# Kernel tuning notes

Hardware: AMD Instinct MI355X
Metric: run time of the kernel (lower is better)

Reference implementation:

```python
import jax, jax.numpy as jnp
import numpy as np

N, P, E, D, OUT = 4096, 2048, 65536, 1024, 128


def _lin(k, fin, fout):
    kw, kb = jax.random.split(k)
    s = 1.0 / np.sqrt(fin)
    return (jax.random.uniform(kw, (fin, fout), jnp.float32, -s, s),
            jax.random.uniform(kb, (fout,), jnp.float32, -s, s))


def setup_inputs() -> dict:
    key = jax.random.key(0)
    ks = jax.random.split(key, 16)
    inst_feat = jax.random.normal(ks[0], (N, D), jnp.float32)
    phra_feat = jax.random.normal(ks[1], (P, D), jnp.float32)
    # unique (subject, object) pairs: the original overwrites duplicates in connection_marker
    pair_ids = jax.random.choice(ks[2], N * N, (E,), replace=False)
    conn_mat = jnp.stack([pair_ids // N, pair_ids % N]).astype(jnp.int32)  # [2, E]
    # every phrase id appears -> exist_phra_id == arange(P), matching original indexing
    phra_clu_idx = jax.random.permutation(ks[3], jnp.arange(E, dtype=jnp.int32) % P)
    p_s_W, p_s_b = _lin(ks[4], 2 * D, OUT)
    s_p_W, s_p_b = _lin(ks[5], 2 * D, OUT)
    p_o_W, p_o_b = _lin(ks[6], 2 * D, OUT)
    o_p_W, o_p_b = _lin(ks[7], 2 * D, OUT)
    inst_w1_W, inst_w1_b = _lin(ks[8], D, D)
    inst_w2_W, inst_w2_b = _lin(ks[9], D, D)
    phra_w1_W, phra_w1_b = _lin(ks[10], D, D)
    phra_w2_W, phra_w2_b = _lin(ks[11], D, D)
    return dict(inst_feat=inst_feat, phra_feat=phra_feat, conn_mat=conn_mat,
                phra_clu_idx=phra_clu_idx,
                p_s_W=p_s_W, p_s_b=p_s_b, p_o_W=p_o_W, p_o_b=p_o_b,
                o_p_W=o_p_W, o_p_b=o_p_b, s_p_W=s_p_W, s_p_b=s_p_b,
                inst_w1_W=inst_w1_W, inst_w1_b=inst_w1_b,
                inst_w2_W=inst_w2_W, inst_w2_b=inst_w2_b,
                phra_w1_W=phra_w1_W, phra_w1_b=phra_w1_b,
                phra_w2_W=phra_w2_W, phra_w2_b=phra_w2_b)


def _gated_msg(src, tgt, W, b):
    # MassageGenerator: gate = sigmoid(relu([src; tgt] @ W + b)).mean(1); msg = src * gate
    gate = jax.nn.sigmoid(jax.nn.relu(jnp.concatenate([src, tgt], axis=1) @ W + b)).mean(axis=1)
    return src * gate[:, None]


def _seg_mean(x, seg, num_segments):
    s = jax.ops.segment_sum(x, seg, num_segments=num_segments)
    c = jax.ops.segment_sum(jnp.ones((x.shape[0],), x.dtype), seg, num_segments=num_segments)
    return s / jnp.maximum(c, 1.0)[:, None]  # zeros where no edges == padded msg


def _refine(msg, tar, w1_W, w1_b, w2_W, w2_b):
    # MassageApply: out = input1 + relu(w1(input1)) + relu(w2(input2)); input1 = summed msg
    return msg + jax.nn.relu(msg @ w1_W + w1_b) + jax.nn.relu(tar @ w2_W + w2_b)


def reference(inst_feat, phra_feat, conn_mat, phra_clu_idx,
              p_s_W, p_s_b, p_o_W, p_o_b, o_p_W, o_p_b, s_p_W, s_p_b,
              inst_w1_W, inst_w1_b, inst_w2_W, inst_w2_b,
              phra_w1_W, phra_w1_b, phra_w2_W, phra_w2_b):
    s_idx, o_idx = conn_mat[0], conn_mat[1]
    subj_f = inst_feat[s_idx]          # [E, D]
    obj_f = inst_feat[o_idx]           # [E, D]
    phr_f = phra_feat[phra_clu_idx]    # [E, D]
    n, p = inst_feat.shape[0], phra_feat.shape[0]
    # phrase -> subject / object messages, mean over each node's incident edges
    p_s = _seg_mean(_gated_msg(phr_f, subj_f, p_s_W, p_s_b), s_idx, n)
    p_o = _seg_mean(_gated_msg(phr_f, obj_f, p_o_W, p_o_b), o_idx, n)
    # object / subject -> phrase messages, mean over edges sharing a cluster id
    o_p = _seg_mean(_gated_msg(obj_f, phr_f, o_p_W, o_p_b), phra_clu_idx, p)
    s_p = _seg_mean(_gated_msg(subj_f, phr_f, s_p_W, s_p_b), phra_clu_idx, p)
    inst_out = _refine((p_o + p_s) * 0.5, inst_feat, inst_w1_W, inst_w1_b, inst_w2_W, inst_w2_b)
    phra_out = _refine((o_p + s_p) * 0.5, phra_feat, phra_w1_W, phra_w1_b, phra_w2_W, phra_w2_b)
    return inst_out, phra_out
```

## Files before the change

kernel.cpp:

```cpp
#include <hip/hip_runtime.h>
#include <math.h>

constexpr int NN  = 4096;
constexpr int PP  = 2048;
constexpr int EE  = 65536;
constexpr int DD  = 1024;
constexpr int OUTF = 128;
constexpr int G4  = 512;

typedef __attribute__((ext_vector_type(8))) short short8v;
typedef __attribute__((ext_vector_type(4))) float f32x4;

__device__ __forceinline__ float sigmoid_relu(float z) {
    z = fmaxf(z, 0.0f);
    return 1.0f / (1.0f + __expf(-z));
}
__device__ __forceinline__ float b2f(ushort u) {
    return __uint_as_float(((unsigned int)u) << 16);
}
__device__ __forceinline__ ushort f2b(float f) {
    unsigned int x = __float_as_uint(f);
    return (ushort)((x + 0x7fffu + ((x >> 16) & 1u)) >> 16);
}
__device__ __forceinline__ unsigned int pack2(float a, float b) {
    return (unsigned int)f2b(a) | ((unsigned int)f2b(b) << 16);
}

#define GLD16(gptr, lptr) \
    __builtin_amdgcn_global_load_lds((__attribute__((address_space(1))) const void*)(gptr), \
                                     (__attribute__((address_space(3))) void*)(lptr), 16, 0, 0)
#define ASM_VMCNT(n) asm volatile("s_waitcnt vmcnt(" #n ")" ::: "memory")
#define BARRIER() do { asm volatile("" ::: "memory"); \
                       __builtin_amdgcn_s_barrier();  \
                       asm volatile("" ::: "memory"); } while (0)

constexpr int NCNT    = 2 * (NN + NN + PP);
constexpr int NB_ZERO = NCNT / 256;
constexpr int NB_F2B  = (NN + PP) * DD / 4 / 256;
constexpr int NB_PACK = G4 * DD / 256;
constexpr int NB_WT   = 4 * (DD / 64) * (DD / 64);

__global__ __launch_bounds__(256) void prep_kernel(
        int* __restrict__ cntBlock,
        const float* __restrict__ instF, const float* __restrict__ phraF,
        ushort* __restrict__ instB, ushort* __restrict__ phraB,
        const float* __restrict__ psW, const float* __restrict__ poW,
        const float* __restrict__ opW, const float* __restrict__ spW,
        const float* __restrict__ psB, const float* __restrict__ poB,
        const float* __restrict__ opB, const float* __restrict__ spB,
        ushort* __restrict__ WiT, ushort* __restrict__ WpT,
        float* __restrict__ biascat,
        const float* __restrict__ W0, const float* __restrict__ W1,
        const float* __restrict__ W2, const float* __restrict__ W3,
        ushort* __restrict__ T0, ushort* __restrict__ T1,
        ushort* __restrict__ T2, ushort* __restrict__ T3) {
    __shared__ float tile[64][65];
    int b = blockIdx.x, t = threadIdx.x;
    if (b < NB_ZERO) {
        cntBlock[b * 256 + t] = 0;
        return;
    }
    b -= NB_ZERO;
    if (b < NB_F2B) {
        int i = b * 256 + t;
        constexpr int na4 = NN * DD / 4;
        if (i < na4) {
            float4 v = ((const float4*)instF)[i];
            ushort4 u; u.x = f2b(v.x); u.y = f2b(v.y); u.z = f2b(v.z); u.w = f2b(v.w);
            ((ushort4*)instB)[i] = u;
        } else {
            int j = i - na4;
            float4 v = ((const float4*)phraF)[j];
            ushort4 u; u.x = f2b(v.x); u.y = f2b(v.y); u.z = f2b(v.z); u.w = f2b(v.w);
            ((ushort4*)phraB)[j] = u;
        }
        return;
    }
    b -= NB_F2B;
    if (b < NB_PACK) {
        int idx = b * 256 + t;
        int n = idx >> 10, k = idx & 1023;
        int g = n >> 7, j = n & 127;
        float wi, wp;
        if (g == 0)      { wi = psW[(size_t)(DD + k) * OUTF + j]; wp = psW[(size_t)k * OUTF + j]; }
        else if (g == 1) { wi = poW[(size_t)(DD + k) * OUTF + j]; wp = poW[(size_t)k * OUTF + j]; }
        else if (g == 2) { wi = opW[(size_t)k * OUTF + j];        wp = opW[(size_t)(DD + k) * OUTF + j]; }
        else             { wi = spW[(size_t)k * OUTF + j];        wp = spW[(size_t)(DD + k) * OUTF + j]; }
        WiT[idx] = f2b(wi);
        WpT[idx] = f2b(wp);
        if (idx < G4) {
            int gg = idx >> 7, jj = idx & 127;
            biascat[idx] = (gg == 0) ? psB[jj] : (gg == 1) ? poB[jj]
                         : (gg == 2) ? opB[jj] : spB[jj];
        }
        return;
    }
    b -= NB_PACK;
    int z = b >> 8, rest = b & 255;
    const float* W = (z == 0) ? W0 : (z == 1) ? W1 : (z == 2) ? W2 : W3;
    ushort*      T = (z == 0) ? T0 : (z == 1) ? T1 : (z == 2) ? T2 : T3;
    int k0 = (rest & 15) * 64, n0 = (rest >> 4) * 64;
    int tx = t & 63, ty = t >> 6;
    #pragma unroll
    for (int i = 0; i < 64; i += 4)
        tile[ty + i][tx] = W[(size_t)(k0 + ty + i) * DD + n0 + tx];
    __syncthreads();
    #pragma unroll
    for (int i = 0; i < 64; i += 4)
        T[(size_t)(n0 + ty + i) * DD + k0 + tx] = f2b(tile[tx][ty + i]);
}

template<int BROWS>
__device__ __forceinline__ void stage_tiles(const ushort* __restrict__ A,
                                            const ushort* __restrict__ BT,
                                            int bm, int bn, int k0,
                                            ushort* Asl, ushort* Bsl, int t) {
    #pragma unroll
    for (int r = 0; r < 4; r++) {
        int ch = r * 256 + t;
        int row = ch >> 3;
        int sw = ((ch & 7) ^ (row & 7)) << 3;
        GLD16(A + (size_t)(bm + row) * DD + k0 + sw, &Asl[ch * 8]);
    }
    #pragma unroll
    for (int r = 0; r < BROWS / 32; r++) {
        int ch = r * 256 + t;
        int row = ch >> 3;
        int sw = ((ch & 7) ^ (row & 7)) << 3;
        GLD16(BT + (size_t)(bn + row) * DD + k0 + sw, &Bsl[ch * 8]);
    }
}

template<int NACC>
__device__ __forceinline__ void compute_tiles(const ushort* Asl, const ushort* Bsl,
                                              f32x4 (&acc)[4][NACC],
                                              int wr, int wc, int lr, int lk) {
    #pragma unroll
    for (int kk = 0; kk < 2; kk++) {
        int ch16 = kk * 4 + lk;
        short8v a[4], b[NACC];
        #pragma unroll
        for (int m = 0; m < 4; m++) {
            int ra = wr + m * 16 + lr;
            a[m] = *(const short8v*)&Asl[ra * 64 + ((ch16 ^ (ra & 7)) << 3)];
        }
        #pragma unroll
        for (int n = 0; n < NACC; n++) {
            int rb = wc + n * 16 + lr;
            b[n] = *(const short8v*)&Bsl[rb * 64 + ((ch16 ^ (rb & 7)) << 3)];
        }
        #pragma unroll
        for (int m = 0; m < 4; m++)
            #pragma unroll
            for (int n = 0; n < NACC; n++)
                acc[m][n] = __builtin_amdgcn_mfma_f32_16x16x32_bf16(a[m], b[n], acc[m][n], 0, 0, 0);
    }
}

__global__ __launch_bounds__(256) void mfma_tables_kernel(
        const ushort* __restrict__ instB, const ushort* __restrict__ WiT,
        const ushort* __restrict__ phraB, const ushort* __restrict__ WpT,
        const float* __restrict__ biascat,
        ushort* __restrict__ TiB, ushort* __restrict__ TpB) {
    __shared__ ushort Asl[2][128 * 64];
    __shared__ ushort Bsl[2][64 * 64];
    int bx = blockIdx.x;
    const ushort *A, *BT; ushort* C; const float* bias;
    if (bx < NN / 128) { A = instB; BT = WiT; C = TiB; bias = nullptr; }
    else { bx -= NN / 128; A = phraB; BT = WpT; C = TpB; bias = biascat; }
    int bm = bx * 128, bn = blockIdx.y * 64;
    int t = threadIdx.x;
    const int lane = t & 63, w = t >> 6;
    const int wr = (w >> 1) * 64, wc = (w & 1) * 32;
    const int lr = lane & 15, lk = lane >> 4;
    f32x4 acc[4][2] = {};

    int cur = 0;
    stage_tiles<64>(A, BT, bm, bn, 0, Asl[0], Bsl[0], t);
    for (int k0 = 0; k0 < DD; k0 += 64) {
        int nxt = cur ^ 1;
        if (k0 + 64 < DD) {
            stage_tiles<64>(A, BT, bm, bn, k0 + 64, Asl[nxt], Bsl[nxt], t);
            ASM_VMCNT(6);
        } else {
            ASM_VMCNT(0);
        }
        BARRIER();
        compute_tiles<2>(Asl[cur], Bsl[cur], acc, wr, wc, lr, lk);
        BARRIER();
        cur = nxt;
    }
    #pragma unroll
    for (int m = 0; m < 4; m++) {
        int row = bm + wr + m * 16 + lk * 4;
        #pragma unroll
        for (int n = 0; n < 2; n++) {
            int col = bn + wc + n * 16 + lr;
            float bv = bias ? bias[col] : 0.f;
            #pragma unroll
            for (int r = 0; r < 4; r++)
                C[(size_t)(row + r) * G4 + col] = f2b(acc[m][n][r] + bv);
        }
    }
}

__global__ __launch_bounds__(256) void mfma_refine_kernel(
        const ushort* __restrict__ imsgB, const ushort* __restrict__ instB,
        const ushort* __restrict__ iw1T, const ushort* __restrict__ iw2T,
        const float* __restrict__ ib1, const float* __restrict__ ib2,
        float* __restrict__ iout,
        const ushort* __restrict__ pmsgB, const ushort* __restrict__ phraB,
        const ushort* __restrict__ pw1T, const ushort* __restrict__ pw2T,
        const float* __restrict__ pb1, const float* __restrict__ pb2,
        float* __restrict__ pout) {
    __shared__ ushort Asl[2][128 * 64];
    __shared__ ushort Bsl[2][64 * 64];
    int bx = blockIdx.x;
    const ushort *Am, *Af, *W1, *W2; const float *b1, *b2; float* out;
    if (bx < NN / 128) {
        Am = imsgB; Af = instB; W1 = iw1T; W2 = iw2T; b1 = ib1; b2 = ib2; out = iout;
    } else {
        bx -= NN / 128;
        Am = pmsgB; Af = phraB; W1 = pw1T; W2 = pw2T; b1 = pb1; b2 = pb2; out = pout;
    }
    int bm = bx * 128, bn = blockIdx.y * 64;
    int t = threadIdx.x;
    const int lane = t & 63, w = t >> 6;
    const int wr = (w >> 1) * 64, wc = (w & 1) * 32;
    const int lr = lane & 15, lk = lane >> 4;
    f32x4 acc1[4][2] = {};
    f32x4 acc2[4][2] = {};

    int cur = 0;
    stage_tiles<64>(Am, W1, bm, bn, 0, Asl[0], Bsl[0], t);
    auto run = [&](const ushort* A, const ushort* B, f32x4 (&acc)[4][2],
                   const ushort* An, const ushort* Bn) {
        for (int k0 = 0; k0 < DD; k0 += 64) {
            int nxt = cur ^ 1;
            if (k0 + 64 < DD) {
                stage_tiles<64>(A, B, bm, bn, k0 + 64, Asl[nxt], Bsl[nxt], t);
                ASM_VMCNT(6);
            } else if (An) {
                stage_tiles<64>(An, Bn, bm, bn, 0, Asl[nxt], Bsl[nxt], t);
                ASM_VMCNT(6);
            } else {
                ASM_VMCNT(0);
            }
            BARRIER();
            compute_tiles<2>(Asl[cur], Bsl[cur], acc, wr, wc, lr, lk);
            BARRIER();
            cur = nxt;
        }
    };
    run(Am, W1, acc1, Af, W2);
    run(Af, W2, acc2, nullptr, nullptr);

    #pragma unroll
    for (int m = 0; m < 4; m++) {
        int row = bm + wr + m * 16 + lk * 4;
        #pragma unroll
        for (int n = 0; n < 2; n++) {
            int col = bn + wc + n * 16 + lr;
            float vb1 = b1[col], vb2 = b2[col];
            #pragma unroll
            for (int r = 0; r < 4; r++) {
                float v = b2f(Am[(size_t)(row + r) * DD + col])
                        + fmaxf(acc1[m][n][r] + vb1, 0.f)
                        + fmaxf(acc2[m][n][r] + vb2, 0.f);
                out[(size_t)(row + r) * DD + col] = v;
            }
        }
    }
}

__global__ void hist_kernel(const int* __restrict__ s_idx, const int* __restrict__ o_idx,
                            const int* __restrict__ c_idx,
                            int* cntS, int* cntO, int* cntC) {
    int e = blockIdx.x * blockDim.x + threadIdx.x;
    if (e >= EE) return;
    atomicAdd(&cntS[s_idx[e]], 1);
    atomicAdd(&cntO[o_idx[e]], 1);
    atomicAdd(&cntC[c_idx[e]], 1);
}

__global__ __launch_bounds__(1024) void scan3_kernel(
        const int* __restrict__ cntS, const int* __restrict__ cntO,
        const int* __restrict__ cntC,
        int* __restrict__ startS, int* __restrict__ startO, int* __restrict__ startC) {
    const int* cnt; int* start; int n;
    if (blockIdx.x == 0)      { cnt = cntS; start = startS; n = NN; }
    else if (blockIdx.x == 1) { cnt = cntO; start = startO; n = NN; }
    else                      { cnt = cntC; start = startC; n = PP; }
    __shared__ int sh[1024];
    int t = threadIdx.x;
    int per = n >> 10;
    int base = t * per;
    int s = 0;
    for (int i = 0; i < per; i++) s += cnt[base + i];
    sh[t] = s;
    __syncthreads();
    for (int off = 1; off < 1024; off <<= 1) {
        int v = (t >= off) ? sh[t - off] : 0;
        __syncthreads();
        sh[t] += v;
        __syncthreads();
    }
    int ex = (t == 0) ? 0 : sh[t - 1];
    for (int i = 0; i < per; i++) { start[base + i] = ex; ex += cnt[base + i]; }
    if (t == 1023) start[n] = ex;
}

__global__ __launch_bounds__(256) void gate_kernel(
        const int* __restrict__ s_idx, const int* __restrict__ o_idx,
        const int* __restrict__ c_idx,
        const int* __restrict__ startS, const int* __restrict__ startO,
        const int* __restrict__ startC,
        int* __restrict__ curS, int* __restrict__ curO, int* __restrict__ curC,
        const ushort* __restrict__ Ti, const ushort* __restrict__ Tp,
        int2* __restrict__ pkS, int2* __restrict__ pkO, int4* __restrict__ pkC) {
    int gid = blockIdx.x * 256 + threadIdx.x;
    int e = gid >> 6, lane = gid & 63;
    if (e >= EE) return;
    int s = s_idx[e], o = o_idx[e], c = c_idx[e];
    const unsigned int* tpc = (const unsigned int*)(Tp + (size_t)c * G4);
    const unsigned int* tis = (const unsigned int*)(Ti + (size_t)s * G4);
    const unsigned int* tio = (const unsigned int*)(Ti + (size_t)o * G4);
    auto pairSig = [](unsigned int a, unsigned int b) {
        float lo = __uint_as_float(a << 16) + __uint_as_float(b << 16);
        float hi = __uint_as_float(a & 0xffff0000u) + __uint_as_float(b & 0xffff0000u);
        return sigmoid_relu(lo) + sigmoid_relu(hi);
    };
    float s0 = pairSig(tpc[lane],       tis[lane]);
    float s1 = pairSig(tpc[64 + lane],  tio[64 + lane]);
    float s2 = pairSig(tpc[128 + lane], tio[128 + lane]);
    float s3 = pairSig(tpc[192 + lane], tis[192 + lane]);
    #pragma unroll
    for (int off = 32; off; off >>= 1) {
        s0 += __shfl_xor(s0, off);
        s1 += __shfl_xor(s1, off);
        s2 += __shfl_xor(s2, off);
        s3 += __shfl_xor(s3, off);
    }
    if (lane == 0) {
        const float inv = 1.0f / 128.0f;
        int ps = startS[s] + atomicAdd(&curS[s], 1);
        int po = startO[o] + atomicAdd(&curO[o], 1);
        int pc = startC[c] + atomicAdd(&curC[c], 1);
        pkS[ps] = make_int2(c, __float_as_int(s0 * inv));
        pkO[po] = make_int2(c, __float_as_int(s1 * inv));
        pkC[pc] = make_int4(o, s, __float_as_int(s2 * inv), __float_as_int(s3 * inv));
    }
}

__device__ __forceinline__ void accum8(float* acc, uint4 v, float g) {
    acc[0] += g * __uint_as_float(v.x << 16);
    acc[1] += g * __uint_as_float(v.x & 0xffff0000u);
    acc[2] += g * __uint_as_float(v.y << 16);
    acc[3] += g * __uint_as_float(v.y & 0xffff0000u);
    acc[4] += g * __uint_as_float(v.z << 16);
    acc[5] += g * __uint_as_float(v.z & 0xffff0000u);
    acc[6] += g * __uint_as_float(v.w << 16);
    acc[7] += g * __uint_as_float(v.w & 0xffff0000u);
}

__global__ __launch_bounds__(256) void seg_kernel(
        const ushort* __restrict__ phraB, const ushort* __restrict__ instB,
        const int2* __restrict__ pkS, const int* __restrict__ startS,
        const int2* __restrict__ pkO, const int* __restrict__ startO,
        const int4* __restrict__ pkC, const int* __restrict__ startC,
        ushort* __restrict__ imsgB, ushort* __restrict__ pmsgB) {
    __shared__ float lds[4][64 * 17];
    int w = threadIdx.x >> 6, lane = threadIdx.x & 63;
    float acc[16];
    #pragma unroll
    for (int j = 0; j < 16; j++) acc[j] = 0.f;
    int bx = blockIdx.x;
    bool instSide = bx < NN / 2;
    int segB, segE;
    ushort* msgB;
    int base2;
    if (instSide) {
        int node = bx * 2 + (w >> 1);
        const int2* pk_list = (w & 1) ? pkO : pkS;
        const int*  start   = (w & 1) ? startO : startS;
        int b = start[node], e = start[node + 1];
        if (b < e) {
            int2 pk = pk_list[b];
            const uint4* r = (const uint4*)(phraB + (size_t)pk.x * DD) + lane;
            uint4 c0 = r[0], c1 = r[64];
            for (int i = b + 1; i < e; i++) {
                int2 pkn = pk_list[i];
                const uint4* rn = (const uint4*)(phraB + (size_t)pkn.x * DD) + lane;
                uint4 n0 = rn[0], n1 = rn[64];
                float g = __int_as_float(pk.y);
                accum8(acc, c0, g); accum8(acc + 8, c1, g);
                pk = pkn; c0 = n0; c1 = n1;
            }
            float g = __int_as_float(pk.y);
            accum8(acc, c0, g); accum8(acc + 8, c1, g);
        }
        segB = b; segE = e; msgB = imsgB; base2 = bx * 2;
    } else {
        int pbx = bx - NN / 2;
        int p = pbx * 2 + (w >> 1);
        int half = w & 1;
        int cb = startC[p], ce = startC[p + 1];
        int i0 = cb + half;
        if (i0 < ce) {
            int4 pk = pkC[i0];
            const uint4* ro = (const uint4*)(instB + (size_t)pk.x * DD) + lane;
            const uint4* rs = (const uint4*)(instB + (size_t)pk.y * DD) + lane;
            uint4 o0 = ro[0], o1 = ro[64], s0 = rs[0], s1 = rs[64];
            for (int i = i0 + 2; i < ce; i += 2) {
                int4 pkn = pkC[i];
                const uint4* rno = (const uint4*)(instB + (size_t)pkn.x * DD) + lane;
                const uint4* rns = (const uint4*)(instB + (size_t)pkn.y * DD) + lane;
                uint4 no0 = rno[0], no1 = rno[64], ns0 = rns[0], ns1 = rns[64];
                float go = __int_as_float(pk.z), gs = __int_as_float(pk.w);
                accum8(acc, o0, go); accum8(acc + 8, o1, go);
                accum8(acc, s0, gs); accum8(acc + 8, s1, gs);
                pk = pkn; o0 = no0; o1 = no1; s0 = ns0; s1 = ns1;
            }
            float go = __int_as_float(pk.z), gs = __int_as_float(pk.w);
            accum8(acc, o0, go); accum8(acc + 8, o1, go);
            accum8(acc, s0, gs); accum8(acc + 8, s1, gs);
        }
        segB = cb; segE = ce; msgB = pmsgB; base2 = pbx * 2;
    }
    float scale = 0.5f / (float)max(segE - segB, 1);
    #pragma unroll
    for (int j = 0; j < 16; j++) lds[w][lane * 17 + j] = acc[j] * scale;
    __syncthreads();
    int u = threadIdx.x & 127;
    int outrow = base2 + (threadIdx.x >> 7);
    int w0 = (threadIdx.x >> 7) << 1;
    int off = (u & 63) * 17 + (u >> 6) * 8;
    float4 a0 = *(const float4*)&lds[w0][off];
    float4 a1 = *(const float4*)&lds[w0][off + 4];
    float4 b0 = *(const float4*)&lds[w0 + 1][off];
    float4 b1 = *(const float4*)&lds[w0 + 1][off + 4];
    uint4 o;
    o.x = pack2(a0.x + b0.x, a0.y + b0.y);
    o.y = pack2(a0.z + b0.z, a0.w + b0.w);
    o.z = pack2(a1.x + b1.x, a1.y + b1.y);
    o.w = pack2(a1.z + b1.z, a1.w + b1.w);
    *(uint4*)&msgB[(size_t)outrow * DD + u * 8] = o;
}

extern "C" void kernel_launch(void* const* d_in, const int* in_sizes, int n_in,
                              void* d_out, int out_size, void* d_ws, size_t ws_size,
                              hipStream_t stream) {
    (void)in_sizes; (void)n_in; (void)out_size; (void)ws_size;
    const float* inst_feat = (const float*)d_in[0];
    const float* phra_feat = (const float*)d_in[1];
    const int*   conn      = (const int*)d_in[2];
    const int*   clu       = (const int*)d_in[3];
    const float* psW = (const float*)d_in[4];  const float* psB = (const float*)d_in[5];
    const float* poW = (const float*)d_in[6];  const float* poB = (const float*)d_in[7];
    const float* opW = (const float*)d_in[8];  const float* opB = (const float*)d_in[9];
    const float* spW = (const float*)d_in[10]; const float* spB = (const float*)d_in[11];
    const float* iw1W = (const float*)d_in[12]; const float* iw1B = (const float*)d_in[13];
    const float* iw2W = (const float*)d_in[14]; const float* iw2B = (const float*)d_in[15];
    const float* pw1W = (const float*)d_in[16]; const float* pw1B = (const float*)d_in[17];
    const float* pw2W = (const float*)d_in[18]; const float* pw2B = (const float*)d_in[19];
    const int* s_idx = conn;
    const int* o_idx = conn + EE;

    char* ws = (char*)d_ws;
    size_t off = 0;
    auto alloc = [&](size_t bytes) {
        char* p = ws + off;
        off += (bytes + 255) & ~(size_t)255;
        return p;
    };
    ushort* instB = (ushort*)alloc((size_t)NN * DD * 2);
    ushort* phraB = (ushort*)alloc((size_t)PP * DD * 2);
    ushort* WiT   = (ushort*)alloc((size_t)G4 * DD * 2);
    ushort* WpT   = (ushort*)alloc((size_t)G4 * DD * 2);
    ushort* iw1T  = (ushort*)alloc((size_t)DD * DD * 2);
    ushort* iw2T  = (ushort*)alloc((size_t)DD * DD * 2);
    ushort* pw1T  = (ushort*)alloc((size_t)DD * DD * 2);
    ushort* pw2T  = (ushort*)alloc((size_t)DD * DD * 2);
    float* biascat = (float*)alloc(G4 * 4);
    ushort* TiB   = (ushort*)alloc((size_t)NN * G4 * 2);
    ushort* TpB   = (ushort*)alloc((size_t)PP * G4 * 2);
    int* cntBlock = (int*)alloc((size_t)NCNT * 4);
    int* cntS = cntBlock;      int* cntO = cntS + NN;  int* cntC = cntO + NN;
    int* curS = cntC + PP;     int* curO = curS + NN;  int* curC = curO + NN;
    int* startS = (int*)alloc((NN + 1) * 4);
    int* startO = (int*)alloc((NN + 1) * 4);
    int* startC = (int*)alloc((PP + 1) * 4);
    int2* pkS   = (int2*)alloc((size_t)EE * 8);
    int2* pkO   = (int2*)alloc((size_t)EE * 8);
    int4* pkC   = (int4*)alloc((size_t)EE * 16);
    ushort* imsgB = (ushort*)alloc((size_t)NN * DD * 2);
    ushort* pmsgB = (ushort*)alloc((size_t)PP * DD * 2);

    float* inst_out = (float*)d_out;
    float* phra_out = inst_out + (size_t)NN * DD;

    prep_kernel<<<NB_ZERO + NB_F2B + NB_PACK + NB_WT, 256, 0, stream>>>(
        cntBlock, inst_feat, phra_feat, instB, phraB,
        psW, poW, opW, spW, psB, poB, opB, spB, WiT, WpT, biascat,
        iw1W, iw2W, pw1W, pw2W, iw1T, iw2T, pw1T, pw2T);

    hist_kernel<<<EE / 256, 256, 0, stream>>>(s_idx, o_idx, clu, cntS, cntO, cntC);
    scan3_kernel<<<3, 1024, 0, stream>>>(cntS, cntO, cntC, startS, startO, startC);

    mfma_tables_kernel<<<dim3((NN + PP) / 128, G4 / 64), 256, 0, stream>>>(
        instB, WiT, phraB, WpT, biascat, TiB, TpB);

    gate_kernel<<<(EE * 64) / 256, 256, 0, stream>>>(
        s_idx, o_idx, clu, startS, startO, startC, curS, curO, curC,
        TiB, TpB, pkS, pkO, pkC);

    seg_kernel<<<NN / 2 + PP / 2, 256, 0, stream>>>(
        phraB, instB, pkS, startS, pkO, startO, pkC, startC, imsgB, pmsgB);

    mfma_refine_kernel<<<dim3((NN + PP) / 128, DD / 64), 256, 0, stream>>>(
        imsgB, instB, iw1T, iw2T, iw1B, iw2B, inst_out,
        pmsgB, phraB, pw1T, pw2T, pw1B, pw2B, phra_out);
}
```

Before: 158.1 us.

## Split segment-mean kernel across feature quarters for four times more blocks

The segment-mean kernel now splits the 1024-wide feature dimension into four 256-wide quarters, each handled by its own block, so the grid grows fourfold. The block index is interleaved so the four quarter-blocks of the same node pair are adjacent and can share cached row data. Each lane now holds 4 accumulators and issues 8-byte loads instead of 16 accumulators with two 16-byte loads, which lowers register pressure and raises occupancy for the latency-bound gather. The cost is four times as many reads of the segment start and packed index arrays, plus smaller per-lane memory transactions.

```diff
diff --git a/kernel.cpp b/kernel.cpp
--- a/kernel.cpp
+++ b/kernel.cpp
@@ -25,6 +25,8 @@
 __device__ __forceinline__ unsigned int pack2(float a, float b) {
     return (unsigned int)f2b(a) | ((unsigned int)f2b(b) << 16);
 }
+__device__ __forceinline__ float lo16(unsigned int u) { return __uint_as_float(u << 16); }
+__device__ __forceinline__ float hi16(unsigned int u) { return __uint_as_float(u & 0xffff0000u); }
 
 #define GLD16(gptr, lptr) \
     __builtin_amdgcn_global_load_lds((__attribute__((address_space(1))) const void*)(gptr), \
@@ -352,15 +354,10 @@
     }
 }
 
-__device__ __forceinline__ void accum8(float* acc, uint4 v, float g) {
-    acc[0] += g * __uint_as_float(v.x << 16);
-    acc[1] += g * __uint_as_float(v.x & 0xffff0000u);
-    acc[2] += g * __uint_as_float(v.y << 16);
-    acc[3] += g * __uint_as_float(v.y & 0xffff0000u);
-    acc[4] += g * __uint_as_float(v.z << 16);
-    acc[5] += g * __uint_as_float(v.z & 0xffff0000u);
-    acc[6] += g * __uint_as_float(v.w << 16);
-    acc[7] += g * __uint_as_float(v.w & 0xffff0000u);
+__device__ __forceinline__ void accum4(float& a0, float& a1, float& a2, float& a3,
+                                       uint2 v, float g) {
+    a0 += g * lo16(v.x); a1 += g * hi16(v.x);
+    a2 += g * lo16(v.y); a3 += g * hi16(v.y);
 }
 
 __global__ __launch_bounds__(256) void seg_kernel(
@@ -369,82 +366,76 @@
         const int2* __restrict__ pkO, const int* __restrict__ startO,
         const int4* __restrict__ pkC, const int* __restrict__ startC,
         ushort* __restrict__ imsgB, ushort* __restrict__ pmsgB) {
-    __shared__ float lds[4][64 * 17];
+    __shared__ float lds[4][64 * 5];
+    int bid = blockIdx.x;
+    int x = bid & 7;
+    int q = x >> 1;
+    int sub = ((bid >> 3) << 1) + (x & 1);
+    int qoff = q * 256;
     int w = threadIdx.x >> 6, lane = threadIdx.x & 63;
-    float acc[16];
-    #pragma unroll
-    for (int j = 0; j < 16; j++) acc[j] = 0.f;
-    int bx = blockIdx.x;
-    bool instSide = bx < NN / 2;
+    float a0 = 0.f, a1 = 0.f, a2 = 0.f, a3 = 0.f;
+    bool instSide = sub < NN / 2;
     int segB, segE;
     ushort* msgB;
     int base2;
     if (instSide) {
-        int node = bx * 2 + (w >> 1);
+        int node = sub * 2 + (w >> 1);
         const int2* pk_list = (w & 1) ? pkO : pkS;
         const int*  start   = (w & 1) ? startO : startS;
         int b = start[node], e = start[node + 1];
         if (b < e) {
             int2 pk = pk_list[b];
-            const uint4* r = (const uint4*)(phraB + (size_t)pk.x * DD) + lane;
-            uint4 c0 = r[0], c1 = r[64];
+            uint2 v = *(const uint2*)(phraB + (size_t)pk.x * DD + qoff + lane * 4);
             for (int i = b + 1; i < e; i++) {
                 int2 pkn = pk_list[i];
-                const uint4* rn = (const uint4*)(phraB + (size_t)pkn.x * DD) + lane;
-                uint4 n0 = rn[0], n1 = rn[64];
-                float g = __int_as_float(pk.y);
-                accum8(acc, c0, g); accum8(acc + 8, c1, g);
-                pk = pkn; c0 = n0; c1 = n1;
+                uint2 vn = *(const uint2*)(phraB + (size_t)pkn.x * DD + qoff + lane * 4);
+                accum4(a0, a1, a2, a3, v, __int_as_float(pk.y));
+                pk = pkn; v = vn;
             }
-            float g = __int_as_float(pk.y);
-            accum8(acc, c0, g); accum8(acc + 8, c1, g);
-        }
-        segB = b; segE = e; msgB = imsgB; base2 = bx * 2;
+            accum4(a0, a1, a2, a3, v, __int_as_float(pk.y));
+        }
+        segB = b; segE = e; msgB = imsgB; base2 = sub * 2;
     } else {
-        int pbx = bx - NN / 2;
+        int pbx = sub - NN / 2;
         int p = pbx * 2 + (w >> 1);
         int half = w & 1;
         int cb = startC[p], ce = startC[p + 1];
         int i0 = cb + half;
         if (i0 < ce) {
             int4 pk = pkC[i0];
-            const uint4* ro = (const uint4*)(instB + (size_t)pk.x * DD) + lane;
-            const uint4* rs = (const uint4*)(instB + (size_t)pk.y * DD) + lane;
-            uint4 o0 = ro[0], o1 = ro[64], s0 = rs[0], s1 = rs[64];
+            uint2 vo = *(const uint2*)(instB + (size_t)pk.x * DD + qoff + lane * 4);
+            uint2 vs = *(const uint2*)(instB + (size_t)pk.y * DD + qoff + lane * 4);
             for (int i = i0 + 2; i < ce; i += 2) {
                 int4 pkn = pkC[i];
-                const uint4* rno = (const uint4*)(instB + (size_t)pkn.x * DD) + lane;
-                const uint4* rns = (const uint4*)(instB + (size_t)pkn.y * DD) + lane;
-                uint4 no0 = rno[0], no1 = rno[64], ns0 = rns[0], ns1 = rns[64];
-                float go = __int_as_float(pk.z), gs = __int_as_float(pk.w);
-                accum8(acc, o0, go); accum8(acc + 8, o1, go);
-                accum8(acc, s0, gs); accum8(acc + 8, s1, gs);
-                pk = pkn; o0 = no0; o1 = no1; s0 = ns0; s1 = ns1;
+                uint2 vno = *(const uint2*)(instB + (size_t)pkn.x * DD + qoff + lane * 4);
+                uint2 vns = *(const uint2*)(instB + (size_t)pkn.y * DD + qoff + lane * 4);
+                accum4(a0, a1, a2, a3, vo, __int_as_float(pk.z));
+                accum4(a0, a1, a2, a3, vs, __int_as_float(pk.w));
+                pk = pkn; vo = vno; vs = vns;
             }
-            float go = __int_as_float(pk.z), gs = __int_as_float(pk.w);
-            accum8(acc, o0, go); accum8(acc + 8, o1, go);
-            accum8(acc, s0, gs); accum8(acc + 8, s1, gs);
+            accum4(a0, a1, a2, a3, vo, __int_as_float(pk.z));
+            accum4(a0, a1, a2, a3, vs, __int_as_float(pk.w));
         }
         segB = cb; segE = ce; msgB = pmsgB; base2 = pbx * 2;
     }
     float scale = 0.5f / (float)max(segE - segB, 1);
-    #pragma unroll
-    for (int j = 0; j < 16; j++) lds[w][lane * 17 + j] = acc[j] * scale;
+    lds[w][lane * 5 + 0] = a0 * scale;
+    lds[w][lane * 5 + 1] = a1 * scale;
+    lds[w][lane * 5 + 2] = a2 * scale;
+    lds[w][lane * 5 + 3] = a3 * scale;
     __syncthreads();
-    int u = threadIdx.x & 127;
-    int outrow = base2 + (threadIdx.x >> 7);
-    int w0 = (threadIdx.x >> 7) << 1;
-    int off = (u & 63) * 17 + (u >> 6) * 8;
-    float4 a0 = *(const float4*)&lds[w0][off];
-    float4 a1 = *(const float4*)&lds[w0][off + 4];
-    float4 b0 = *(const float4*)&lds[w0 + 1][off];
-    float4 b1 = *(const float4*)&lds[w0 + 1][off + 4];
-    uint4 o;
-    o.x = pack2(a0.x + b0.x, a0.y + b0.y);
-    o.y = pack2(a0.z + b0.z, a0.w + b0.w);
-    o.z = pack2(a1.x + b1.x, a1.y + b1.y);
-    o.w = pack2(a1.z + b1.z, a1.w + b1.w);
-    *(uint4*)&msgB[(size_t)outrow * DD + u * 8] = o;
+    if (threadIdx.x < 128) {
+        int node = threadIdx.x >> 6, l = threadIdx.x & 63;
+        int w0 = node * 2;
+        float s0 = lds[w0][l * 5 + 0] + lds[w0 + 1][l * 5 + 0];
+        float s1 = lds[w0][l * 5 + 1] + lds[w0 + 1][l * 5 + 1];
+        float s2 = lds[w0][l * 5 + 2] + lds[w0 + 1][l * 5 + 2];
+        float s3 = lds[w0][l * 5 + 3] + lds[w0 + 1][l * 5 + 3];
+        uint2 o;
+        o.x = pack2(s0, s1);
+        o.y = pack2(s2, s3);
+        *(uint2*)&msgB[(size_t)(base2 + node) * DD + qoff + l * 4] = o;
+    }
 }
 
 extern "C" void kernel_launch(void* const* d_in, const int* in_sizes, int n_in,
@@ -514,7 +505,7 @@
         s_idx, o_idx, clu, startS, startO, startC, curS, curO, curC,
         TiB, TpB, pkS, pkO, pkC);
 
-    seg_kernel<<<NN / 2 + PP / 2, 256, 0, stream>>>(
+    seg_kernel<<<(NN / 2 + PP / 2) * 4, 256, 0, stream>>>(
         phraB, instB, pkS, startS, pkO, startO, pkC, startC, imsgB, pmsgB);
 
     mfma_refine_kernel<<<dim3((NN + PP) / 128, DD / 64), 256, 0, stream>>>(
```

Measured after the change: 174.5 us. 10.4% more time.
